# Performance work log

Hardware: AMD Instinct MI355X
Metric: run time of the kernel (lower is better)

## Reference

```python
import jax, jax.numpy as jnp
import numpy as np

GLYPH_DIM = 4096
PADDING_IDX = GLYPH_DIM  # 4096
GLYPH_EMB = 20           # CHAR_EMB 16 + COLOR_EMB 4
HIDDEN = 32
MAX_LEN = 64


def setup_inputs() -> dict:
    key = jax.random.key(0)
    k1, k2, k3, k4, k5, k6, k7 = jax.random.split(key, 7)
    B, H, W = 8192, 21, 79
    glyph_chars = jax.random.randint(k1, (B, H, W), 0, 256, dtype=jnp.int32)
    glyph_colors = jax.random.randint(k2, (B, H, W), 0, 16, dtype=jnp.int32)
    # Embedding table with zero padding row (torch padding_idx semantics)
    emb_table = jax.random.normal(k3, (GLYPH_DIM + 1, GLYPH_EMB), dtype=jnp.float32) * 0.02
    emb_table = emb_table.at[PADDING_IDX].set(0.0)
    s = 1.0 / np.sqrt(HIDDEN)
    W_ih = jax.random.uniform(k4, (HIDDEN, GLYPH_EMB), minval=-s, maxval=s, dtype=jnp.float32)
    W_hh = jax.random.uniform(k5, (HIDDEN, HIDDEN), minval=-s, maxval=s, dtype=jnp.float32)
    b_ih = jax.random.uniform(k6, (HIDDEN,), minval=-s, maxval=s, dtype=jnp.float32)
    b_hh = jax.random.uniform(k7, (HIDDEN,), minval=-s, maxval=s, dtype=jnp.float32)
    return {"glyph_chars": glyph_chars, "glyph_colors": glyph_colors,
            "emb_table": emb_table, "W_ih": W_ih, "W_hh": W_hh,
            "b_ih": b_ih, "b_hh": b_hh}


def _encode_bag(glyph_chars, glyph_colors):
    """Batched sorted-unique compaction over the bounded glyph id range."""
    B = glyph_chars.shape[0]
    g_ids = ((glyph_chars << 4) + glyph_colors).reshape(B, -1)  # [B, H*W]
    # presence[b, g] = glyph g appears in sample b (batched histogram)
    bidx = jnp.broadcast_to(jnp.arange(B, dtype=g_ids.dtype)[:, None], g_ids.shape)
    presence = jnp.zeros((B, GLYPH_DIM), dtype=bool).at[bidx, g_ids].set(True)
    # compact: present ids keep their value, absent become PADDING_IDX (=4096),
    # so sorting yields ascending unique ids followed by padding.
    ids = jnp.arange(GLYPH_DIM, dtype=jnp.int32)
    keys = jnp.where(presence, ids, jnp.int32(PADDING_IDX))
    bag = jnp.sort(keys, axis=1)[:, :MAX_LEN]  # [B, MAX_LEN]
    lengths = jnp.minimum(presence.sum(axis=1), MAX_LEN)  # [B]
    return bag, lengths


def reference(glyph_chars, glyph_colors, emb_table, W_ih, W_hh, b_ih, b_hh):
    bag, lengths = _encode_bag(glyph_chars, glyph_colors)
    emb = emb_table[bag]  # [B, MAX_LEN, GLYPH_EMB]
    B = emb.shape[0]

    # packed RNN == plain RNN where hidden state freezes past each sequence length
    xs = jnp.swapaxes(emb, 0, 1)  # [T, B, E]

    def step(h, inp):
        xt, t = inp
        h_new = jnp.tanh(xt @ W_ih.T + b_ih + h @ W_hh.T + b_hh)
        h = jnp.where((t < lengths)[:, None], h_new, h)
        return h, None

    h0 = jnp.zeros((B, HIDDEN), dtype=emb.dtype)
    h, _ = jax.lax.scan(step, h0, (xs, jnp.arange(MAX_LEN)))
    return (h, emb, bag)
```

## Files before the change

### kernel.cpp

```cpp
#include <hip/hip_runtime.h>

#define HW 1659
#define PADID 4096
#define EMB 20
#define HID 32
#define MAXLEN 64
#define PROJ_BLOCKS 128

typedef float v2f __attribute__((ext_vector_type(2)));
typedef float v4f __attribute__((ext_vector_type(4)));

template <int CTRL>
__device__ __forceinline__ float dppf(float v) {
    return __builtin_bit_cast(float,
        __builtin_amdgcn_update_dpp(0, __builtin_bit_cast(int, v),
                                    CTRL, 0xF, 0xF, true));
}
#define DPP_XOR1 0xB1
#define DPP_XOR2 0x4E
#define DPP_XOR7 0x141
#define DPP_XORF 0x140

__global__ __launch_bounds__(128, 4) void bag_emb_kernel(
    const int* __restrict__ chars, const int* __restrict__ colors,
    const float* __restrict__ emb_table, const float* __restrict__ W_ih,
    float* __restrict__ out_emb, float* __restrict__ out_bag,
    float* __restrict__ proj, int nbag)
{
    const int tid = threadIdx.x;

    if ((int)blockIdx.x >= nbag) {
        const int gid = ((int)blockIdx.x - nbag) * 128 + tid;
        const int NP = (PADID + 1) * HID;
        for (int idx = gid; idx < NP; idx += PROJ_BLOCKS * 128) {
            const int g = idx >> 5, j = idx & 31;
            const float* er = emb_table + (size_t)g * EMB;
            const float* wr = W_ih + j * EMB;
            float s = 0.f;
#pragma unroll
            for (int k = 0; k < EMB; k++) s += wr[k] * er[k];
            proj[idx] = s;
        }
        return;
    }

    __shared__ __align__(16) unsigned char pres[4096];
    __shared__ int bagl[64];
    __shared__ int wsum[2];

    const int lane = tid & 63;
    const int wv   = tid >> 6;
    const int b    = blockIdx.x;

    const int base = b * HW;
    const int pe = (4 - (base & 3)) & 3;
    const int nv = (HW - pe) >> 2;
    const int nt = HW - pe - (nv << 2);
    const int4* c4 = (const int4*)(chars + base + pe);
    const int4* k4 = (const int4*)(colors + base + pe);

    int4 ca0 = c4[tid],       ka0 = k4[tid];
    int4 ca1 = c4[tid + 128], ka1 = k4[tid + 128];
    int4 ca2 = c4[tid + 256], ka2 = k4[tid + 256];
    const bool has3 = (tid + 384) < nv;
    const int i3 = has3 ? tid + 384 : tid;
    int4 ca3 = c4[i3], ka3 = k4[i3];
    int gp = -1, gt = -1;
    if (tid < pe) gp = (chars[base + tid] << 4) + colors[base + tid];
    if (tid < nt) {
        const int i = base + pe + (nv << 2) + tid;
        gt = (chars[i] << 4) + colors[i];
    }

    ((uint4*)pres)[tid]       = make_uint4(0u, 0u, 0u, 0u);
    ((uint4*)pres)[tid + 128] = make_uint4(0u, 0u, 0u, 0u);
    if (tid < 64) bagl[tid] = PADID;
    __syncthreads();

    pres[(ca0.x << 4) + ka0.x] = 1;
    pres[(ca0.y << 4) + ka0.y] = 1;
    pres[(ca0.z << 4) + ka0.z] = 1;
    pres[(ca0.w << 4) + ka0.w] = 1;
    pres[(ca1.x << 4) + ka1.x] = 1;
    pres[(ca1.y << 4) + ka1.y] = 1;
    pres[(ca1.z << 4) + ka1.z] = 1;
    pres[(ca1.w << 4) + ka1.w] = 1;
    pres[(ca2.x << 4) + ka2.x] = 1;
    pres[(ca2.y << 4) + ka2.y] = 1;
    pres[(ca2.z << 4) + ka2.z] = 1;
    pres[(ca2.w << 4) + ka2.w] = 1;
    if (has3) {
        pres[(ca3.x << 4) + ka3.x] = 1;
        pres[(ca3.y << 4) + ka3.y] = 1;
        pres[(ca3.z << 4) + ka3.z] = 1;
        pres[(ca3.w << 4) + ka3.w] = 1;
    }
    if (gp >= 0) pres[gp] = 1;
    if (gt >= 0) pres[gt] = 1;
    __syncthreads();

    const unsigned M = 0x01010101u;
    int base_cnt = 0;
#pragma unroll 1
    for (int r = 0; r < 2; r++) {
        const uint4 w = ((const uint4*)pres)[tid + (r << 7)];
        const int cnt = __popc(w.x & M) + __popc(w.y & M)
                      + __popc(w.z & M) + __popc(w.w & M);
        int pre = cnt;
#pragma unroll
        for (int d = 1; d < 64; d <<= 1) {
            const int v = __shfl_up(pre, d, 64);
            if (lane >= d) pre += v;
        }
        if (lane == 63) wsum[wv] = pre;
        __syncthreads();
        const int w0 = wsum[0], w1 = wsum[1];
        int p = base_cnt + (wv ? w0 : 0) + pre - cnt;
        if (p < 64) {
            const unsigned wrd[4] = {w.x, w.y, w.z, w.w};
            const int idbase = (r << 11) + (tid << 4);
#pragma unroll
            for (int c = 0; c < 4; c++) {
#pragma unroll
                for (int k = 0; k < 4; k++) {
                    if ((wrd[c] >> (8 * k)) & 1) {
                        if (p < 64) bagl[p] = idbase + 4 * c + k;
                        p++;
                    }
                }
            }
        }
        base_cnt += w0 + w1;
        if (base_cnt >= 64) break;
        __syncthreads();
    }
    __syncthreads();

    if (tid < 64) out_bag[(size_t)b * 64 + tid] = (float)bagl[tid];

    const float4* tab4 = (const float4*)emb_table;
    float4* dst4 = (float4*)(out_emb + (size_t)b * (MAXLEN * EMB));
#pragma unroll
    for (int m = 0; m < 3; m++) {
        const int q = tid + (m << 7);
        if (q < MAXLEN * 5) {
            const int t = q / 5;
            const int mm = q - t * 5;
            const int row = bagl[t];
            dst4[q] = tab4[row * 5 + mm];
        }
    }
}


__device__ __forceinline__ void rnn_step(
    float idxv, v2f pv,
    const v2f (&w0)[16], const v2f (&w1)[16],
    float sb0, float sb1, float& h0, float& h1)
{
    const bool upd = idxv < 4095.5f;

    v2f g[16];
    g[0] = (v2f){h0, h1};
    g[1] = (v2f){dppf<DPP_XOR1>(g[0][0]), dppf<DPP_XOR1>(g[0][1])};
    g[2] = (v2f){dppf<DPP_XOR2>(g[0][0]), dppf<DPP_XOR2>(g[0][1])};
    g[3] = (v2f){dppf<DPP_XOR2>(g[1][0]), dppf<DPP_XOR2>(g[1][1])};
#pragma unroll
    for (int m = 0; m < 4; m++)
        g[4 + m] = (v2f){dppf<DPP_XOR7>(g[m][0]), dppf<DPP_XOR7>(g[m][1])};
#pragma unroll
    for (int m = 0; m < 8; m++)
        g[8 + m] = (v2f){dppf<DPP_XORF>(g[m][0]), dppf<DPP_XORF>(g[m][1])};

    v2f a0 = (v2f){0.f, 0.f}, b0 = a0, a1 = a0, b1 = a0;
#pragma unroll
    for (int m = 0; m < 16; m += 2) {
        a0 = __builtin_elementwise_fma(w0[m],     g[m],     a0);
        b0 = __builtin_elementwise_fma(w0[m + 1], g[m + 1], b0);
        a1 = __builtin_elementwise_fma(w1[m],     g[m],     a1);
        b1 = __builtin_elementwise_fma(w1[m + 1], g[m + 1], b1);
    }
    float s0 = sb0 + pv[0] + (a0[0] + a0[1]) + (b0[0] + b0[1]);
    float s1 = sb1 + pv[1] + (a1[0] + a1[1]) + (b1[0] + b1[1]);

    float e0 = __expf(2.f * s0);
    float e1 = __expf(2.f * s1);
    float th0 = 1.f - 2.f * __builtin_amdgcn_rcpf(e0 + 1.f);
    float th1 = 1.f - 2.f * __builtin_amdgcn_rcpf(e1 + 1.f);

    h0 = upd ? th0 : h0;
    h1 = upd ? th1 : h1;
}

__global__ __launch_bounds__(128, 2)
void rnn_kernel(
    const float* __restrict__ proj, const float* __restrict__ bagf,
    const float* __restrict__ W_hh,
    const float* __restrict__ b_ih, const float* __restrict__ b_hh,
    float* __restrict__ out_h)
{
    const int tid  = threadIdx.x;
    const int wv   = tid >> 6;
    const int lane = tid & 63;
    const int sl   = lane >> 4;
    const int ib   = wv * 4 + sl;
    const int jj   = lane & 15;
    const int b    = blockIdx.x * 8 + ib;

    const int GMAP[16] = {0,1,2,3, 7,6,5,4, 15,14,13,12,11,10,9,8};

    v2f w0[16], w1[16];
    const v2f* wr0 = (const v2f*)(W_hh + (2 * jj) * HID);
    const v2f* wr1 = (const v2f*)(W_hh + (2 * jj + 1) * HID);
#pragma unroll
    for (int m = 0; m < 16; m++) {
        const int c = jj ^ GMAP[m];
        w0[m] = wr0[c];
        w1[m] = wr1[c];
    }
    const float sb0 = b_ih[2 * jj]     + b_hh[2 * jj];
    const float sb1 = b_ih[2 * jj + 1] + b_hh[2 * jj + 1];

    const v2f* proj2 = (const v2f*)proj;
    const float* bp = bagf + (size_t)b * 64;
    const v4f* bp4 = (const v4f*)bp;

    float h0 = 0.f, h1 = 0.f;

    float idxA[8], idxB[8];
    v2f pvA[8], pvB[8];

    {
        v4f q0 = bp4[0], q1 = bp4[1];
        idxA[0] = q0[0]; idxA[1] = q0[1]; idxA[2] = q0[2]; idxA[3] = q0[3];
        idxA[4] = q1[0]; idxA[5] = q1[1]; idxA[6] = q1[2]; idxA[7] = q1[3];
#pragma unroll
        for (int i = 0; i < 8; i++)
            pvA[i] = proj2[(int)idxA[i] * 16 + jj];
        v4f q2 = bp4[2], q3 = bp4[3];
        idxB[0] = q2[0]; idxB[1] = q2[1]; idxB[2] = q2[2]; idxB[3] = q2[3];
        idxB[4] = q3[0]; idxB[5] = q3[1]; idxB[6] = q3[2]; idxB[7] = q3[3];
    }

#pragma unroll 1
    for (int c = 0; c < 64; c += 16) {
        const int nc = (c + 16) & 63;

#pragma unroll
        for (int i = 0; i < 8; i++)
            pvB[i] = proj2[(int)idxB[i] * 16 + jj];

#pragma unroll
        for (int i = 0; i < 8; i++)
            rnn_step(idxA[i], pvA[i], w0, w1, sb0, sb1, h0, h1);

        {
            const v4f qa0 = bp4[(nc >> 2) + 0], qa1 = bp4[(nc >> 2) + 1];
            idxA[0] = qa0[0]; idxA[1] = qa0[1]; idxA[2] = qa0[2]; idxA[3] = qa0[3];
            idxA[4] = qa1[0]; idxA[5] = qa1[1]; idxA[6] = qa1[2]; idxA[7] = qa1[3];
        }

#pragma unroll
        for (int i = 0; i < 8; i++)
            rnn_step(idxB[i], pvB[i], w0, w1, sb0, sb1, h0, h1);

#pragma unroll
        for (int i = 0; i < 8; i++)
            pvA[i] = proj2[(int)idxA[i] * 16 + jj];

        {
            const v4f qb0 = bp4[(nc >> 2) + 2], qb1 = bp4[(nc >> 2) + 3];
            idxB[0] = qb0[0]; idxB[1] = qb0[1]; idxB[2] = qb0[2]; idxB[3] = qb0[3];
            idxB[4] = qb1[0]; idxB[5] = qb1[1]; idxB[6] = qb1[2]; idxB[7] = qb1[3];
        }
    }

    ((float2*)(out_h + (size_t)b * HID))[jj] = make_float2(h0, h1);
}

__global__ __launch_bounds__(128, 4) void rnn_kernel_noproj(
    const float* __restrict__ emb, const float* __restrict__ bagf,
    const float* __restrict__ W_ih, const float* __restrict__ W_hh,
    const float* __restrict__ b_ih, const float* __restrict__ b_hh,
    float* __restrict__ out_h)
{
    __shared__ float hbuf[4][32];
    const int tid = threadIdx.x;
    const int ib  = tid >> 5;
    const int j   = tid & 31;
    const int b   = blockIdx.x * 4 + ib;

    float wih[EMB];
#pragma unroll
    for (int k = 0; k < EMB; k++) wih[k] = W_ih[j * EMB + k];
    float whh[HID];
#pragma unroll
    for (int k = 0; k < HID; k++) whh[k] = W_hh[j * HID + k];
    const float sbias = b_ih[j] + b_hh[j];

    const float* bp = bagf + (size_t)b * 64;
    unsigned long long m0 = __ballot(bp[j]      < 4095.5f);
    unsigned long long m1 = __ballot(bp[32 + j] < 4095.5f);
    const int half = ib & 1;
    const int len = __popc((unsigned)(m0 >> (half * 32)))
                  + __popc((unsigned)(m1 >> (half * 32)));

    hbuf[ib][j] = 0.f;
    asm volatile("s_waitcnt lgkmcnt(0)" ::: "memory");

    float h = 0.f;
    const float* xb = emb + (size_t)b * (MAXLEN * EMB);
    for (int t = 0; t < MAXLEN; t++) {
        const float4* xp = (const float4*)(xb + t * EMB);
        float4 x0 = xp[0], x1 = xp[1], x2 = xp[2], x3 = xp[3], x4 = xp[4];
        float s = sbias;
        const float4* hb4 = (const float4*)hbuf[ib];
#pragma unroll
        for (int m = 0; m < 8; m++) {
            float4 hv = hb4[m];
            s += whh[4*m+0]*hv.x + whh[4*m+1]*hv.y
               + whh[4*m+2]*hv.z + whh[4*m+3]*hv.w;
        }
        s += wih[0]*x0.x + wih[1]*x0.y + wih[2]*x0.z + wih[3]*x0.w;
        s += wih[4]*x1.x + wih[5]*x1.y + wih[6]*x1.z + wih[7]*x1.w;
        s += wih[8]*x2.x + wih[9]*x2.y + wih[10]*x2.z + wih[11]*x2.w;
        s += wih[12]*x3.x + wih[13]*x3.y + wih[14]*x3.z + wih[15]*x3.w;
        s += wih[16]*x4.x + wih[17]*x4.y + wih[18]*x4.z + wih[19]*x4.w;
        s = fminf(fmaxf(s, -9.f), 9.f);
        float e = __expf(2.f * s);
        float th = (e - 1.f) * __builtin_amdgcn_rcpf(e + 1.f);
        h = (t < len) ? th : h;
        hbuf[ib][j] = h;
        asm volatile("s_waitcnt lgkmcnt(0)" ::: "memory");
    }
    out_h[(size_t)b * HID + j] = h;
}

extern "C" void kernel_launch(void* const* d_in, const int* in_sizes, int n_in,
                              void* d_out, int out_size, void* d_ws, size_t ws_size,
                              hipStream_t stream) {
    const int*   chars     = (const int*)d_in[0];
    const int*   colors    = (const int*)d_in[1];
    const float* emb_table = (const float*)d_in[2];
    const float* W_ih      = (const float*)d_in[3];
    const float* W_hh      = (const float*)d_in[4];
    const float* b_ih      = (const float*)d_in[5];
    const float* b_hh      = (const float*)d_in[6];

    const int B = in_sizes[0] / HW;

    float* out     = (float*)d_out;
    float* out_h   = out;
    float* out_emb = out + (size_t)B * HID;
    float* out_bag = out_emb + (size_t)B * MAXLEN * EMB;

    const size_t proj_bytes = (size_t)(PADID + 1) * HID * sizeof(float);

    if (ws_size >= proj_bytes && (B % 8) == 0) {
        float* proj = (float*)d_ws;
        bag_emb_kernel<<<B + PROJ_BLOCKS, 128, 0, stream>>>(
            chars, colors, emb_table, W_ih, out_emb, out_bag, proj, B);
        rnn_kernel<<<B / 8, 128, 0, stream>>>(proj, out_bag, W_hh, b_ih, b_hh, out_h);
    } else {
        bag_emb_kernel<<<B, 128, 0, stream>>>(
            chars, colors, emb_table, W_ih, out_emb, out_bag, (float*)d_ws, B);
        rnn_kernel_noproj<<<B / 4, 128, 0, stream>>>(out_emb, out_bag, W_ih, W_hh,
                                                     b_ih, b_hh, out_h);
    }
}
```

Baseline: 192.0 us.

## Prefetch all projected rows into LDS via async global_load_lds before RNN recurrence

The RNN kernel now uses one wave per block (4 samples) and, before the recurrence, issues async global-to-LDS loads for all 64 timesteps' projected input rows into two 16KB shared arrays. It then runs the 64-step recurrence reading inputs from LDS, with the update mask computed from a counted length instead of per-step index comparisons. This replaces the software-pipelined register double buffering of gathered projections and aims to take global-load latency off the serial dependency chain. The cost is 32KB of LDS per block, which limits occupancy, and no overlap of loads with compute within a block.

Measured after the change: 206.8 us. 7.7% more time.

```diff
diff --git a/kernel.cpp b/kernel.cpp
--- a/kernel.cpp
+++ b/kernel.cpp
@@ -8,7 +8,6 @@
 #define PROJ_BLOCKS 128
 
 typedef float v2f __attribute__((ext_vector_type(2)));
-typedef float v4f __attribute__((ext_vector_type(4)));
 
 template <int CTRL>
 __device__ __forceinline__ float dppf(float v) {
@@ -154,12 +153,10 @@
 
 
 __device__ __forceinline__ void rnn_step(
-    float idxv, v2f pv,
+    bool upd, v2f pv,
     const v2f (&w0)[16], const v2f (&w1)[16],
     float sb0, float sb1, float& h0, float& h1)
 {
-    const bool upd = idxv < 4095.5f;
-
     v2f g[16];
     g[0] = (v2f){h0, h1};
     g[1] = (v2f){dppf<DPP_XOR1>(g[0][0]), dppf<DPP_XOR1>(g[0][1])};
@@ -192,20 +189,20 @@
     h1 = upd ? th1 : h1;
 }
 
-__global__ __launch_bounds__(128, 2)
+__global__ __launch_bounds__(64, 2)
 void rnn_kernel(
     const float* __restrict__ proj, const float* __restrict__ bagf,
     const float* __restrict__ W_hh,
     const float* __restrict__ b_ih, const float* __restrict__ b_hh,
     float* __restrict__ out_h)
 {
-    const int tid  = threadIdx.x;
-    const int wv   = tid >> 6;
-    const int lane = tid & 63;
+    __shared__ float pvx[MAXLEN * 64];
+    __shared__ float pvy[MAXLEN * 64];
+
+    const int lane = threadIdx.x & 63;
     const int sl   = lane >> 4;
-    const int ib   = wv * 4 + sl;
     const int jj   = lane & 15;
-    const int b    = blockIdx.x * 8 + ib;
+    const int b    = blockIdx.x * 4 + sl;
 
     const int GMAP[16] = {0,1,2,3, 7,6,5,4, 15,14,13,12,11,10,9,8};
 
@@ -221,58 +218,37 @@
     const float sb0 = b_ih[2 * jj]     + b_hh[2 * jj];
     const float sb1 = b_ih[2 * jj + 1] + b_hh[2 * jj + 1];
 
-    const v2f* proj2 = (const v2f*)proj;
-    const float* bp = bagf + (size_t)b * 64;
-    const v4f* bp4 = (const v4f*)bp;
+    const float* bps = bagf + (size_t)b * 64;
+
+    int len = 0;
+#pragma unroll 1
+    for (int ch = 0; ch < 4; ++ch) {
+        float id16[16];
+#pragma unroll
+        for (int i = 0; i < 16; ++i) id16[i] = bps[ch * 16 + i];
+#pragma unroll
+        for (int i = 0; i < 16; ++i) {
+            const int t   = ch * 16 + i;
+            const int row = (int)id16[i];
+            len += (row < PADID) ? 1 : 0;
+            const float* src = proj + row * HID + (jj << 1);
+            __builtin_amdgcn_global_load_lds(
+                (const __attribute__((address_space(1))) void*)src,
+                (__attribute__((address_space(3))) void*)&pvx[t << 6],
+                4, 0, 0);
+            __builtin_amdgcn_global_load_lds(
+                (const __attribute__((address_space(1))) void*)src,
+                (__attribute__((address_space(3))) void*)&pvy[t << 6],
+                4, 4, 0);
+        }
+    }
+    asm volatile("s_waitcnt vmcnt(0)" ::: "memory");
 
     float h0 = 0.f, h1 = 0.f;
-
-    float idxA[8], idxB[8];
-    v2f pvA[8], pvB[8];
-
-    {
-        v4f q0 = bp4[0], q1 = bp4[1];
-        idxA[0] = q0[0]; idxA[1] = q0[1]; idxA[2] = q0[2]; idxA[3] = q0[3];
-        idxA[4] = q1[0]; idxA[5] = q1[1]; idxA[6] = q1[2]; idxA[7] = q1[3];
-#pragma unroll
-        for (int i = 0; i < 8; i++)
-            pvA[i] = proj2[(int)idxA[i] * 16 + jj];
-        v4f q2 = bp4[2], q3 = bp4[3];
-        idxB[0] = q2[0]; idxB[1] = q2[1]; idxB[2] = q2[2]; idxB[3] = q2[3];
-        idxB[4] = q3[0]; idxB[5] = q3[1]; idxB[6] = q3[2]; idxB[7] = q3[3];
-    }
-
-#pragma unroll 1
-    for (int c = 0; c < 64; c += 16) {
-        const int nc = (c + 16) & 63;
-
-#pragma unroll
-        for (int i = 0; i < 8; i++)
-            pvB[i] = proj2[(int)idxB[i] * 16 + jj];
-
-#pragma unroll
-        for (int i = 0; i < 8; i++)
-            rnn_step(idxA[i], pvA[i], w0, w1, sb0, sb1, h0, h1);
-
-        {
-            const v4f qa0 = bp4[(nc >> 2) + 0], qa1 = bp4[(nc >> 2) + 1];
-            idxA[0] = qa0[0]; idxA[1] = qa0[1]; idxA[2] = qa0[2]; idxA[3] = qa0[3];
-            idxA[4] = qa1[0]; idxA[5] = qa1[1]; idxA[6] = qa1[2]; idxA[7] = qa1[3];
-        }
-
-#pragma unroll
-        for (int i = 0; i < 8; i++)
-            rnn_step(idxB[i], pvB[i], w0, w1, sb0, sb1, h0, h1);
-
-#pragma unroll
-        for (int i = 0; i < 8; i++)
-            pvA[i] = proj2[(int)idxA[i] * 16 + jj];
-
-        {
-            const v4f qb0 = bp4[(nc >> 2) + 2], qb1 = bp4[(nc >> 2) + 3];
-            idxB[0] = qb0[0]; idxB[1] = qb0[1]; idxB[2] = qb0[2]; idxB[3] = qb0[3];
-            idxB[4] = qb1[0]; idxB[5] = qb1[1]; idxB[6] = qb1[2]; idxB[7] = qb1[3];
-        }
+#pragma unroll 4
+    for (int t = 0; t < MAXLEN; ++t) {
+        const v2f pv = (v2f){ pvx[(t << 6) + lane], pvy[(t << 6) + lane] };
+        rnn_step(t < len, pv, w0, w1, sb0, sb1, h0, h1);
     }
 
     ((float2*)(out_h + (size_t)b * HID))[jj] = make_float2(h0, h1);
@@ -356,11 +332,11 @@
 
     const size_t proj_bytes = (size_t)(PADID + 1) * HID * sizeof(float);
 
-    if (ws_size >= proj_bytes && (B % 8) == 0) {
+    if (ws_size >= proj_bytes && (B % 4) == 0) {
         float* proj = (float*)d_ws;
         bag_emb_kernel<<<B + PROJ_BLOCKS, 128, 0, stream>>>(
             chars, colors, emb_table, W_ih, out_emb, out_bag, proj, B);
-        rnn_kernel<<<B / 8, 128, 0, stream>>>(proj, out_bag, W_hh, b_ih, b_hh, out_h);
+        rnn_kernel<<<B / 4, 64, 0, stream>>>(proj, out_bag, W_hh, b_ih, b_hh, out_h);
     } else {
         bag_emb_kernel<<<B, 128, 0, stream>>>(
             chars, colors, emb_table, W_ih, out_emb, out_bag, (float*)d_ws, B);
```
